# Kernel tuning notes

Hardware: AMD Instinct MI355X
Metric: run time of the kernel (lower is better)

The kernel has to match this reference:

```python
import jax, jax.numpy as jnp
import numpy as np

EPS = 1e-5
N_HEAD = 16


def layernorm(x, g, b):
    mu = jnp.mean(x, axis=-1, keepdims=True)
    var = jnp.mean(jnp.square(x - mu), axis=-1, keepdims=True)
    return (x - mu) * jax.lax.rsqrt(var + EPS) * g + b


def setup_inputs() -> dict:
    key = jax.random.key(0)
    ks = jax.random.split(key, 8)
    B, S, D = 4, 2048, 1024
    F = 4 * D
    s = 0.02
    return {
        "h": jax.random.normal(ks[0], (B, S, D), jnp.float32),
        "ln1_g": jnp.ones((D,), jnp.float32),
        "ln1_b": jnp.zeros((D,), jnp.float32),
        "wq": jax.random.normal(ks[1], (D, D), jnp.float32) * s,
        "bq": jnp.zeros((D,), jnp.float32),
        "wk": jax.random.normal(ks[2], (D, D), jnp.float32) * s,
        "bk": jnp.zeros((D,), jnp.float32),
        "wv": jax.random.normal(ks[3], (D, D), jnp.float32) * s,
        "bv": jnp.zeros((D,), jnp.float32),
        "wo": jax.random.normal(ks[4], (D, D), jnp.float32) * s,
        "bo": jnp.zeros((D,), jnp.float32),
        "ln2_g": jnp.ones((D,), jnp.float32),
        "ln2_b": jnp.zeros((D,), jnp.float32),
        "wfc": jax.random.normal(ks[5], (F, D), jnp.float32) * s,
        "bfc": jnp.zeros((F,), jnp.float32),
        "wproj": jax.random.normal(ks[6], (D, F), jnp.float32) * s,
        "bproj": jnp.zeros((D,), jnp.float32),
    }


def reference(h, ln1_g, ln1_b, wq, bq, wk, bk, wv, bv, wo, bo,
              ln2_g, ln2_b, wfc, bfc, wproj, bproj):
    B, S, D = h.shape
    H = N_HEAD
    Dh = D // H

    # --- attention sub-block ---
    r = h
    x = layernorm(h, ln1_g, ln1_b)
    q = (x @ wq.T + bq).reshape(B, S, H, Dh)
    k = (x @ wk.T + bk).reshape(B, S, H, Dh)
    v = (x @ wv.T + bv).reshape(B, S, H, Dh)

    scores = jnp.einsum("bqhd,bkhd->bhqk", q, k) / jnp.sqrt(jnp.float32(Dh))
    causal = jnp.tril(jnp.ones((S, S), bool))  # [S,S]
    scores = jnp.where(causal, scores, jnp.finfo(scores.dtype).min)
    probs = jax.nn.softmax(scores, axis=-1)
    o = jnp.einsum("bhqk,bkhd->bqhd", probs, v).reshape(B, S, D)
    h = r + (o @ wo.T + bo)

    # --- MLP sub-block ---
    r = h
    x = layernorm(h, ln2_g, ln2_b)
    x = jax.nn.gelu(x @ wfc.T + bfc, approximate=True)  # NewGELU (tanh)
    h = r + (x @ wproj.T + bproj)
    return h
```

## Files before the change

kernel.cpp:

```cpp
#include <hip/hip_runtime.h>
#include <hip/hip_bf16.h>
#include <stdint.h>


typedef short bf16x8 __attribute__((ext_vector_type(8)));
typedef float f32x4  __attribute__((ext_vector_type(4)));
typedef float f32x16 __attribute__((ext_vector_type(16)));
typedef short s16x4  __attribute__((ext_vector_type(4)));

__device__ __forceinline__ short f2bf(float f) {
  union { float f; uint32_t u; } a;
  a.f = f;
  uint32_t r = a.u + 0x7fffu + ((a.u >> 16) & 1u);
  return (short)(r >> 16);
}

__device__ __forceinline__ unsigned cvt_pk_bf16(float lo, float hi_) {
  unsigned r;
  asm("v_cvt_pk_bf16_f32 %0, %1, %2" : "=v"(r) : "v"(lo), "v"(hi_));
  return r;
}

__device__ __forceinline__ void gload_lds16(const void* g, void* l) {
  __builtin_amdgcn_global_load_lds(
      (const __attribute__((address_space(1))) void*)g,
      (__attribute__((address_space(3))) void*)l, 16, 0, 0);
}

__device__ __forceinline__ float gelu_f(float x) {
  float y = 0.7978845608028654f * (x + 0.044715f * x * x * x);
  y = fminf(fmaxf(y, -20.f), 20.f);
  float e = __expf(2.f * y);
  return 0.5f * x * (1.f + (e - 1.f) / (e + 1.f));
}

__global__ __launch_bounds__(256)
void cvt_f32_bf16(const float* __restrict__ in, short* __restrict__ out, int n4) {
  int i = blockIdx.x * 256 + threadIdx.x;
  if (i < n4) {
    float4 v = ((const float4*)in)[i];
    s16x4 o;
    o[0] = f2bf(v.x); o[1] = f2bf(v.y); o[2] = f2bf(v.z); o[3] = f2bf(v.w);
    ((s16x4*)out)[i] = o;
  }
}

__global__ __launch_bounds__(256)
void ln_fwd(const float* __restrict__ x, const float* __restrict__ g,
            const float* __restrict__ b, short* __restrict__ y) {
  const long row = blockIdx.x;
  const int t = threadIdx.x;
  const float4 xv = ((const float4*)(x + row * 1024))[t];
  float s  = xv.x + xv.y + xv.z + xv.w;
  float ss = xv.x * xv.x + xv.y * xv.y + xv.z * xv.z + xv.w * xv.w;
#pragma unroll
  for (int m = 1; m < 64; m <<= 1) {
    s  += __shfl_xor(s, m);
    ss += __shfl_xor(ss, m);
  }
  __shared__ float rs[4], rss[4];
  const int wid = t >> 6, lane = t & 63;
  if (lane == 0) { rs[wid] = s; rss[wid] = ss; }
  __syncthreads();
  s  = rs[0] + rs[1] + rs[2] + rs[3];
  ss = rss[0] + rss[1] + rss[2] + rss[3];
  const float mu   = s * (1.f / 1024.f);
  const float var  = ss * (1.f / 1024.f) - mu * mu;
  const float rstd = rsqrtf(var + 1e-5f);
  const float4 gv = ((const float4*)g)[t];
  const float4 bv = ((const float4*)b)[t];
  s16x4 ov;
  ov[0] = f2bf((xv.x - mu) * rstd * gv.x + bv.x);
  ov[1] = f2bf((xv.y - mu) * rstd * gv.y + bv.y);
  ov[2] = f2bf((xv.z - mu) * rstd * gv.z + bv.z);
  ov[3] = f2bf((xv.w - mu) * rstd * gv.w + bv.w);
  *(s16x4*)(y + row * 1024 + t * 4) = ov;
}

template <int OUT_BF16, int HAS_RES, int HAS_GELU>
__global__ __launch_bounds__(512, 2)
void gemm_bt2(const short* __restrict__ A, const short* __restrict__ W,
              const float* __restrict__ bias, const float* __restrict__ res,
              void* __restrict__ out, int M, int N, int K) {
  __shared__ short As[2][128 * 64];
  __shared__ short Bs[2][256 * 64];
  const int tid = threadIdx.x;
  const int wid = tid >> 6, lane = tid & 63;
  const int l16 = lane & 15, lg = lane >> 4;
  const int wm = wid >> 2, wn = wid & 3;

  const int nbx = N >> 8;
  const int nwg = nbx * (M >> 7);
  int flat = (int)blockIdx.x;
  if ((nwg & 7) == 0) flat = (flat & 7) * (nwg >> 3) + (flat >> 3);
  const int brow = (flat / nbx) * 128, bcol = (flat % nbx) * 256;

  f32x4 acc[4][4] = {};

  const int r0 = tid >> 3, g0 = tid & 7;

  auto STAGE = [&](int buf, int kt) {
#pragma unroll
    for (int i = 0; i < 2; ++i) {
      const int row = i * 64 + r0;
      gload_lds16(A + (long)(brow + row) * K + kt + 8 * (g0 ^ (row & 7)),
                  &As[buf][(i * 512 + wid * 64) * 8]);
    }
#pragma unroll
    for (int i = 0; i < 4; ++i) {
      const int row = i * 64 + r0;
      gload_lds16(W + (long)(bcol + row) * K + kt + 8 * (g0 ^ (row & 7)),
                  &Bs[buf][(i * 512 + wid * 64) * 8]);
    }
  };

  const int NT = K >> 6;
  STAGE(0, 0);
  STAGE(1, 64);

  for (int t = 0; t < NT; ++t) {
    const int cur = t & 1;
    if (t < NT - 1) asm volatile("s_waitcnt vmcnt(6)" ::: "memory");
    else            asm volatile("s_waitcnt vmcnt(0)" ::: "memory");
    __builtin_amdgcn_s_barrier();

    bf16x8 af0[4], af1[4], bf0[4], bf1[4];
#pragma unroll
    for (int m = 0; m < 4; ++m) {
      const int r = wm * 64 + m * 16 + l16;
      af0[m] = *(const bf16x8*)&As[cur][r * 64 + 8 * (lg ^ (r & 7))];
      af1[m] = *(const bf16x8*)&As[cur][r * 64 + 8 * ((4 + lg) ^ (r & 7))];
    }
#pragma unroll
    for (int n = 0; n < 4; ++n) {
      const int r = wn * 64 + n * 16 + l16;
      bf0[n] = *(const bf16x8*)&Bs[cur][r * 64 + 8 * (lg ^ (r & 7))];
      bf1[n] = *(const bf16x8*)&Bs[cur][r * 64 + 8 * ((4 + lg) ^ (r & 7))];
    }

    __builtin_amdgcn_s_setprio(1);
#pragma unroll
    for (int m = 0; m < 4; ++m)
#pragma unroll
      for (int n = 0; n < 4; ++n)
        acc[m][n] = __builtin_amdgcn_mfma_f32_16x16x32_bf16(af0[m], bf0[n], acc[m][n], 0, 0, 0);
    __builtin_amdgcn_s_setprio(0);

    asm volatile("s_waitcnt lgkmcnt(0)" ::: "memory");
    __builtin_amdgcn_s_barrier();
    if (t + 2 < NT) STAGE(cur, (t + 2) * 64);

    __builtin_amdgcn_s_setprio(1);
#pragma unroll
    for (int m = 0; m < 4; ++m)
#pragma unroll
      for (int n = 0; n < 4; ++n)
        acc[m][n] = __builtin_amdgcn_mfma_f32_16x16x32_bf16(af1[m], bf1[n], acc[m][n], 0, 0, 0);
    __builtin_amdgcn_s_setprio(0);
  }

#pragma unroll
  for (int n = 0; n < 4; ++n) {
    const int col = bcol + wn * 64 + n * 16 + l16;
    const float bb = bias[col];
#pragma unroll
    for (int m = 0; m < 4; ++m) {
#pragma unroll
      for (int j = 0; j < 4; ++j) {
        const long row = brow + wm * 64 + m * 16 + lg * 4 + j;
        float vv = acc[m][n][j] + bb;
        if (HAS_GELU) vv = gelu_f(vv);
        if (HAS_RES) vv += res[row * N + col];
        if (OUT_BF16) ((short*)out)[row * N + col] = f2bf(vv);
        else          ((float*)out)[row * N + col] = vv;
      }
    }
  }
}

__global__ __launch_bounds__(256)
void transpose_v(const short* __restrict__ v, short* __restrict__ vtg,
                 int S, int ldv, int H) {
  __shared__ short t[64][66];
  const int bh = blockIdx.y, b = bh / H, hh = bh % H;
  const int s0 = blockIdx.x * 64;
  const int tid = threadIdx.x;
#pragma unroll
  for (int i = 0; i < 2; ++i) {
    const int c = i * 256 + tid;
    const int sl = c >> 3, d8 = (c & 7) * 8;
    bf16x8 vv = *(const bf16x8*)&v[((long)b * S + s0 + sl) * ldv + hh * 64 + d8];
#pragma unroll
    for (int j = 0; j < 8; ++j) t[d8 + j][sl] = vv[j];
  }
  __syncthreads();
#pragma unroll
  for (int i = 0; i < 2; ++i) {
    const int c = i * 256 + tid;
    const int dl = c >> 3, s8 = (c & 7) * 8;
    bf16x8 ov;
#pragma unroll
    for (int j = 0; j < 8; ++j) ov[j] = t[dl][s8 + j];
    *(bf16x8*)&vtg[((long)bh * 64 + dl) * S + s0 + s8] = ov;
  }
}

__global__ __launch_bounds__(256, 4)
void attn_fwd2(const short* __restrict__ qg, const short* __restrict__ kg,
               const short* __restrict__ vtg, short* __restrict__ og,
               int S, int ldq, int D, int H) {
  const int tid = threadIdx.x, wid = tid >> 6, lane = tid & 63;
  const int l31 = lane & 31, hi = lane >> 5;
  const int fid = blockIdx.x;
  const int bh = fid & 63;
  const int b = bh / H, hh = bh % H;
  static const int perm[16] = {15, 0, 8, 7, 1, 14, 6, 9, 13, 2, 10, 5, 3, 12, 4, 11};
  const int qt = perm[(fid >> 6) & 15];
  const int q0 = qt * 128;
  const long qbase = (long)b * S * ldq + hh * 64;
  const long obase = (long)b * S * D + hh * 64;
  const long vbase = (long)bh * 64 * S;

  __shared__ short Ks[2][64 * 64];
  __shared__ short Vs[2][64 * 64];

  auto STAGE = [&](int buf, int k0) {
#pragma unroll
    for (int i = 0; i < 2; ++i) {
      const int c = i * 256 + tid;
      const int row = c >> 3, gl = c & 7;
      gload_lds16(&kg[qbase + (long)(k0 + row) * ldq + 8 * (gl ^ (row & 7))],
                  &Ks[buf][(i * 256 + wid * 64) * 8]);
      gload_lds16(&vtg[vbase + (long)row * S + k0 + 8 * (gl ^ (row & 7))],
                  &Vs[buf][(i * 256 + wid * 64) * 8]);
    }
  };

  const float kScale = 0.125f * 1.44269504089f;

  const int qw = q0 + wid * 32;
  const int qv = qw + l31;

  bf16x8 qf[4];
#pragma unroll
  for (int s = 0; s < 4; ++s)
    qf[s] = *(const bf16x8*)&qg[qbase + (long)qv * ldq + 16 * s + 8 * hi];

  f32x16 oa[2] = {};
  float mr = -3000.f, lr = 0.f;

  const int ntiles = qt * 2 + 2;

  STAGE(0, 0);
  for (int t = 0; t < ntiles; ++t) {
    const int cur = t & 1;
    const int k0 = t * 64;
    if (t + 1 < ntiles) {
      STAGE(cur ^ 1, k0 + 64);
      asm volatile("s_waitcnt vmcnt(4)" ::: "memory");
    } else {
      asm volatile("s_waitcnt vmcnt(0)" ::: "memory");
    }
    __builtin_amdgcn_s_barrier();

    if (k0 < qw + 32) {
      f32x16 st[2] = {};
#pragma unroll
      for (int s = 0; s < 4; ++s) {
        const int g = ((s << 1) | hi) ^ (l31 & 7);
        bf16x8 kf0 = *(const bf16x8*)&Ks[cur][l31 * 64 + 8 * g];
        bf16x8 kf1 = *(const bf16x8*)&Ks[cur][(32 + l31) * 64 + 8 * g];
        st[0] = __builtin_amdgcn_mfma_f32_32x32x16_bf16(kf0, qf[s], st[0], 0, 0, 0);
        st[1] = __builtin_amdgcn_mfma_f32_32x32x16_bf16(kf1, qf[s], st[1], 0, 0, 0);
      }

      const bool need_mask = (k0 + 63 > qw);
      float pv[2][16];
#pragma unroll
      for (int kb = 0; kb < 2; ++kb)
#pragma unroll
        for (int r = 0; r < 16; ++r) {
          float v = st[kb][r] * kScale;
          if (need_mask) {
            const int key = k0 + kb * 32 + (r & 3) + 8 * (r >> 2) + 4 * hi;
            if (key > qv) v = -1e30f;
          }
          pv[kb][r] = v;
        }

      float t8[8];
#pragma unroll
      for (int j = 0; j < 8; ++j)
        t8[j] = fmaxf(fmaxf(pv[0][j], pv[0][8 + j]), fmaxf(pv[1][j], pv[1][8 + j]));
      float rm = fmaxf(fmaxf(fmaxf(t8[0], t8[1]), fmaxf(t8[2], t8[3])),
                       fmaxf(fmaxf(t8[4], t8[5]), fmaxf(t8[6], t8[7])));
      rm = fmaxf(rm, __shfl_xor(rm, 32));

      const bool defer = (bool)__all(rm <= mr + 8.f);
      const float mn = defer ? mr : fmaxf(mr, rm);

      float a0 = 0.f, a1 = 0.f, a2 = 0.f, a3 = 0.f;
#pragma unroll
      for (int r = 0; r < 8; ++r) {
        float p0 = exp2f(pv[0][r] - mn);      pv[0][r] = p0;      a0 += p0;
        float p1 = exp2f(pv[0][8 + r] - mn);  pv[0][8 + r] = p1;  a1 += p1;
        float p2 = exp2f(pv[1][r] - mn);      pv[1][r] = p2;      a2 += p2;
        float p3 = exp2f(pv[1][8 + r] - mn);  pv[1][8 + r] = p3;  a3 += p3;
      }
      float ls = (a0 + a1) + (a2 + a3);
      ls += __shfl_xor(ls, 32);

      if (!defer) {
        const float alpha = exp2f(mr - mn);
        lr = lr * alpha + ls;
        mr = mn;
#pragma unroll
        for (int r = 0; r < 16; ++r) {
          const int crow = (r & 3) + 8 * (r >> 2) + 4 * hi;
          const float ar = __shfl(alpha, crow | (lane & 32));
          oa[0][r] *= ar;
          oa[1][r] *= ar;
        }
      } else {
        lr += ls;
      }

      bf16x8 pa[4];
#pragma unroll
      for (int kb = 0; kb < 2; ++kb) {
        unsigned pk[8], ex[8];
#pragma unroll
        for (int i2 = 0; i2 < 8; ++i2)
          pk[i2] = cvt_pk_bf16(pv[kb][2 * i2], pv[kb][2 * i2 + 1]);
#pragma unroll
        for (int i2 = 0; i2 < 8; ++i2)
          ex[i2] = (unsigned)__shfl_xor((int)pk[i2], 32);
        union { unsigned u[4]; bf16x8 v8; } f0, f1;
        f0.u[0] = hi ? ex[2] : pk[0];
        f0.u[1] = hi ? ex[3] : pk[1];
        f0.u[2] = hi ? pk[2] : ex[0];
        f0.u[3] = hi ? pk[3] : ex[1];
        f1.u[0] = hi ? ex[6] : pk[4];
        f1.u[1] = hi ? ex[7] : pk[5];
        f1.u[2] = hi ? pk[6] : ex[4];
        f1.u[3] = hi ? pk[7] : ex[5];
        pa[2 * kb]     = f0.v8;
        pa[2 * kb + 1] = f1.v8;
      }

#pragma unroll
      for (int s = 0; s < 4; ++s) {
        const int g = ((s << 1) | hi) ^ (l31 & 7);
        bf16x8 vf0 = *(const bf16x8*)&Vs[cur][l31 * 64 + 8 * g];
        bf16x8 vf1 = *(const bf16x8*)&Vs[cur][(32 + l31) * 64 + 8 * g];
        oa[0] = __builtin_amdgcn_mfma_f32_32x32x16_bf16(pa[s], vf0, oa[0], 0, 0, 0);
        oa[1] = __builtin_amdgcn_mfma_f32_32x32x16_bf16(pa[s], vf1, oa[1], 0, 0, 0);
      }
    }

    asm volatile("s_waitcnt lgkmcnt(0)" ::: "memory");
    __builtin_amdgcn_s_barrier();
  }

  const float linv = 1.f / lr;
#pragma unroll
  for (int r = 0; r < 16; ++r) {
    const int crow = (r & 3) + 8 * (r >> 2) + 4 * hi;
    const float li = __shfl(linv, crow | (lane & 32));
    const long row = qw + crow;
    og[obase + row * D + l31]      = f2bf(oa[0][r] * li);
    og[obase + row * D + 32 + l31] = f2bf(oa[1][r] * li);
  }
}

extern "C" void kernel_launch(void* const* d_in, const int* in_sizes, int n_in,
                              void* d_out, int out_size, void* d_ws, size_t ws_size,
                              hipStream_t stream) {
  (void)in_sizes; (void)n_in; (void)out_size; (void)ws_size;
  const float* h     = (const float*)d_in[0];
  const float* ln1_g = (const float*)d_in[1];
  const float* ln1_b = (const float*)d_in[2];
  const float* wq    = (const float*)d_in[3];
  const float* bq    = (const float*)d_in[4];
  const float* wk    = (const float*)d_in[5];
  const float* bk    = (const float*)d_in[6];
  const float* wv    = (const float*)d_in[7];
  const float* bv    = (const float*)d_in[8];
  const float* wo    = (const float*)d_in[9];
  const float* bo    = (const float*)d_in[10];
  const float* ln2_g = (const float*)d_in[11];
  const float* ln2_b = (const float*)d_in[12];
  const float* wfc   = (const float*)d_in[13];
  const float* bfc   = (const float*)d_in[14];
  const float* wproj = (const float*)d_in[15];
  const float* bproj = (const float*)d_in[16];

  const int B = 4, S = 2048, D = 1024, H = 16, F = 4096, T = B * S;
  const int D3 = 3 * D;

  char* ws = (char*)d_ws;
  size_t off = 0;
  auto alloc = [&](size_t bytes) {
    void* p = ws + off;
    off += (bytes + 255) & ~(size_t)255;
    return p;
  };
  short* xb   = (short*)alloc((size_t)T * D * 2);
  short* qkv  = (short*)alloc((size_t)T * D3 * 2);
  short* ob   = (short*)alloc((size_t)T * D * 2);
  float* h2   = (float*)alloc((size_t)T * D * 4);
  short* wqkvb  = (short*)alloc((size_t)D3 * D * 2);
  short* wob    = (short*)alloc((size_t)D * D * 2);
  short* wfcb   = (short*)alloc((size_t)F * D * 2);
  short* wprojb = (short*)alloc((size_t)D * F * 2);
  float* bqkv   = (float*)alloc((size_t)D3 * 4);
  short* ub  = qkv;
  short* vtg = (short*)h2;

  cvt_f32_bf16<<<dim3(D * D / 4 / 256), 256, 0, stream>>>(wq, wqkvb, D * D / 4);
  cvt_f32_bf16<<<dim3(D * D / 4 / 256), 256, 0, stream>>>(wk, wqkvb + (size_t)D * D, D * D / 4);
  cvt_f32_bf16<<<dim3(D * D / 4 / 256), 256, 0, stream>>>(wv, wqkvb + (size_t)2 * D * D, D * D / 4);
  cvt_f32_bf16<<<dim3(D * D / 4 / 256), 256, 0, stream>>>(wo, wob, D * D / 4);
  cvt_f32_bf16<<<dim3(F * D / 4 / 256), 256, 0, stream>>>(wfc, wfcb, F * D / 4);
  cvt_f32_bf16<<<dim3(D * F / 4 / 256), 256, 0, stream>>>(wproj, wprojb, D * F / 4);
  hipMemcpyAsync(bqkv,            bq, D * 4, hipMemcpyDeviceToDevice, stream);
  hipMemcpyAsync(bqkv + D,        bk, D * 4, hipMemcpyDeviceToDevice, stream);
  hipMemcpyAsync(bqkv + 2 * D,    bv, D * 4, hipMemcpyDeviceToDevice, stream);

  ln_fwd<<<dim3(T), 256, 0, stream>>>(h, ln1_g, ln1_b, xb);
  gemm_bt2<1, 0, 0><<<dim3((T / 128) * (D3 / 256)), 512, 0, stream>>>(
      xb, wqkvb, bqkv, nullptr, qkv, T, D3, D);
  transpose_v<<<dim3(S / 64, B * H), 256, 0, stream>>>(qkv + 2 * D, vtg, S, D3, H);
  attn_fwd2<<<dim3((S / 128) * (B * H / 64) * 64), 256, 0, stream>>>(
      qkv, qkv + D, vtg, ob, S, D3, D, H);
  gemm_bt2<0, 1, 0><<<dim3((T / 128) * (D / 256)), 512, 0, stream>>>(
      ob, wob, bo, h, h2, T, D, D);

  ln_fwd<<<dim3(T), 256, 0, stream>>>(h2, ln2_g, ln2_b, xb);
  gemm_bt2<1, 0, 1><<<dim3((T / 128) * (F / 256)), 512, 0, stream>>>(
      xb, wfcb, bfc, nullptr, ub, T, F, D);
  gemm_bt2<0, 1, 0><<<dim3((T / 128) * (D / 256)), 512, 0, stream>>>(
      ub, wprojb, bproj, h2, (float*)d_out, T, D, F);
}
```

Before: 415.6 us.

## Switch GEMM to triple-buffered K=32 stages with higher occupancy target

The GEMM K-tile shrinks from 64 to 32 and LDS staging moves from double to triple buffering, with the next-next tile issued at the start of each iteration. The launch bound now targets 4 workgroups per CU instead of 2, since LDS per block drops from 96KB to 72KB. The aim is to deepen prefetch and raise occupancy to hide global-load latency. In exchange there are twice as many barrier-synchronised iterations with half the MFMA work each, and register pressure rises under the tighter launch bound.

```diff
diff --git a/kernel.cpp b/kernel.cpp
--- a/kernel.cpp
+++ b/kernel.cpp
@@ -78,12 +78,12 @@
 }
 
 template <int OUT_BF16, int HAS_RES, int HAS_GELU>
-__global__ __launch_bounds__(512, 2)
-void gemm_bt2(const short* __restrict__ A, const short* __restrict__ W,
+__global__ __launch_bounds__(512, 4)
+void gemm_bt3(const short* __restrict__ A, const short* __restrict__ W,
               const float* __restrict__ bias, const float* __restrict__ res,
               void* __restrict__ out, int M, int N, int K) {
-  __shared__ short As[2][128 * 64];
-  __shared__ short Bs[2][256 * 64];
+  __shared__ short As[3][128 * 32];
+  __shared__ short Bs[3][256 * 32];
   const int tid = threadIdx.x;
   const int wid = tid >> 6, lane = tid & 63;
   const int l16 = lane & 15, lg = lane >> 4;
@@ -97,45 +97,46 @@
 
   f32x4 acc[4][4] = {};
 
-  const int r0 = tid >> 3, g0 = tid & 7;
+  const int r0 = tid >> 2, g0 = tid & 3;
 
   auto STAGE = [&](int buf, int kt) {
+    gload_lds16(A + (long)(brow + r0) * K + kt + 8 * (g0 ^ (r0 & 3)),
+                &As[buf][tid * 8]);
 #pragma unroll
     for (int i = 0; i < 2; ++i) {
-      const int row = i * 64 + r0;
-      gload_lds16(A + (long)(brow + row) * K + kt + 8 * (g0 ^ (row & 7)),
-                  &As[buf][(i * 512 + wid * 64) * 8]);
-    }
-#pragma unroll
-    for (int i = 0; i < 4; ++i) {
-      const int row = i * 64 + r0;
-      gload_lds16(W + (long)(bcol + row) * K + kt + 8 * (g0 ^ (row & 7)),
-                  &Bs[buf][(i * 512 + wid * 64) * 8]);
+      const int row = i * 128 + r0;
+      gload_lds16(W + (long)(bcol + row) * K + kt + 8 * (g0 ^ (row & 3)),
+                  &Bs[buf][(i * 512 + tid) * 8]);
     }
   };
 
-  const int NT = K >> 6;
+  const int NT = K >> 5;
   STAGE(0, 0);
-  STAGE(1, 64);
-
+  STAGE(1, 32);
+
+  int cur = 0;
   for (int t = 0; t < NT; ++t) {
-    const int cur = t & 1;
-    if (t < NT - 1) asm volatile("s_waitcnt vmcnt(6)" ::: "memory");
-    else            asm volatile("s_waitcnt vmcnt(0)" ::: "memory");
+    if (t + 2 < NT) {
+      int sb = cur + 2; if (sb >= 3) sb -= 3;
+      STAGE(sb, (t + 2) * 32);
+      asm volatile("s_waitcnt vmcnt(6)" ::: "memory");
+    } else if (t + 1 < NT) {
+      asm volatile("s_waitcnt vmcnt(3)" ::: "memory");
+    } else {
+      asm volatile("s_waitcnt vmcnt(0)" ::: "memory");
+    }
     __builtin_amdgcn_s_barrier();
 
-    bf16x8 af0[4], af1[4], bf0[4], bf1[4];
+    bf16x8 af[4], bf[4];
 #pragma unroll
     for (int m = 0; m < 4; ++m) {
       const int r = wm * 64 + m * 16 + l16;
-      af0[m] = *(const bf16x8*)&As[cur][r * 64 + 8 * (lg ^ (r & 7))];
-      af1[m] = *(const bf16x8*)&As[cur][r * 64 + 8 * ((4 + lg) ^ (r & 7))];
+      af[m] = *(const bf16x8*)&As[cur][r * 32 + 8 * (lg ^ (r & 3))];
     }
 #pragma unroll
     for (int n = 0; n < 4; ++n) {
       const int r = wn * 64 + n * 16 + l16;
-      bf0[n] = *(const bf16x8*)&Bs[cur][r * 64 + 8 * (lg ^ (r & 7))];
-      bf1[n] = *(const bf16x8*)&Bs[cur][r * 64 + 8 * ((4 + lg) ^ (r & 7))];
+      bf[n] = *(const bf16x8*)&Bs[cur][r * 32 + 8 * (lg ^ (r & 3))];
     }
 
     __builtin_amdgcn_s_setprio(1);
@@ -143,20 +144,12 @@
     for (int m = 0; m < 4; ++m)
 #pragma unroll
       for (int n = 0; n < 4; ++n)
-        acc[m][n] = __builtin_amdgcn_mfma_f32_16x16x32_bf16(af0[m], bf0[n], acc[m][n], 0, 0, 0);
+        acc[m][n] = __builtin_amdgcn_mfma_f32_16x16x32_bf16(af[m], bf[n], acc[m][n], 0, 0, 0);
     __builtin_amdgcn_s_setprio(0);
 
     asm volatile("s_waitcnt lgkmcnt(0)" ::: "memory");
     __builtin_amdgcn_s_barrier();
-    if (t + 2 < NT) STAGE(cur, (t + 2) * 64);
-
-    __builtin_amdgcn_s_setprio(1);
-#pragma unroll
-    for (int m = 0; m < 4; ++m)
-#pragma unroll
-      for (int n = 0; n < 4; ++n)
-        acc[m][n] = __builtin_amdgcn_mfma_f32_16x16x32_bf16(af1[m], bf1[n], acc[m][n], 0, 0, 0);
-    __builtin_amdgcn_s_setprio(0);
+    cur = (cur + 1 == 3) ? 0 : cur + 1;
   }
 
 #pragma unroll
@@ -428,17 +421,17 @@
   hipMemcpyAsync(bqkv + 2 * D,    bv, D * 4, hipMemcpyDeviceToDevice, stream);
 
   ln_fwd<<<dim3(T), 256, 0, stream>>>(h, ln1_g, ln1_b, xb);
-  gemm_bt2<1, 0, 0><<<dim3((T / 128) * (D3 / 256)), 512, 0, stream>>>(
+  gemm_bt3<1, 0, 0><<<dim3((T / 128) * (D3 / 256)), 512, 0, stream>>>(
       xb, wqkvb, bqkv, nullptr, qkv, T, D3, D);
   transpose_v<<<dim3(S / 64, B * H), 256, 0, stream>>>(qkv + 2 * D, vtg, S, D3, H);
   attn_fwd2<<<dim3((S / 128) * (B * H / 64) * 64), 256, 0, stream>>>(
       qkv, qkv + D, vtg, ob, S, D3, D, H);
-  gemm_bt2<0, 1, 0><<<dim3((T / 128) * (D / 256)), 512, 0, stream>>>(
+  gemm_bt3<0, 1, 0><<<dim3((T / 128) * (D / 256)), 512, 0, stream>>>(
       ob, wob, bo, h, h2, T, D, D);
 
   ln_fwd<<<dim3(T), 256, 0, stream>>>(h2, ln2_g, ln2_b, xb);
-  gemm_bt2<1, 0, 1><<<dim3((T / 128) * (F / 256)), 512, 0, stream>>>(
+  gemm_bt3<1, 0, 1><<<dim3((T / 128) * (F / 256)), 512, 0, stream>>>(
       xb, wfcb, bfc, nullptr, ub, T, F, D);
-  gemm_bt2<0, 1, 0><<<dim3((T / 128) * (D / 256)), 512, 0, stream>>>(
+  gemm_bt3<0, 1, 0><<<dim3((T / 128) * (D / 256)), 512, 0, stream>>>(
       ub, wprojb, bproj, h2, (float*)d_out, T, D, F);
 }
```

Result: slower. 440.2 us (+5.9%).

## Triple-buffer GEMM LDS staging and interleave global loads with MFMA halves

Applied to the files above, without the earlier changes.

The GEMM kernel moves from a double-buffered to a triple-buffered LDS pipeline. Global-to-LDS loads for tile t+2 are split across the two MFMA half-steps, with barriers and sched_barrier pinning the order so load issue overlaps compute. Fragment loads are reduced to one set of registers reused across both K halves. Launch bounds drop from 2 to 1 workgroup per CU because LDS use grows to 144KB, trading occupancy for a deeper prefetch pipeline.

```diff
diff --git a/kernel.cpp b/kernel.cpp
--- a/kernel.cpp
+++ b/kernel.cpp
@@ -78,12 +78,12 @@
 }
 
 template <int OUT_BF16, int HAS_RES, int HAS_GELU>
-__global__ __launch_bounds__(512, 2)
-void gemm_bt2(const short* __restrict__ A, const short* __restrict__ W,
+__global__ __launch_bounds__(512, 1)
+void gemm_bt4(const short* __restrict__ A, const short* __restrict__ W,
               const float* __restrict__ bias, const float* __restrict__ res,
               void* __restrict__ out, int M, int N, int K) {
-  __shared__ short As[2][128 * 64];
-  __shared__ short Bs[2][256 * 64];
+  __shared__ short As[3][128 * 64];
+  __shared__ short Bs[3][256 * 64];
   const int tid = threadIdx.x;
   const int wid = tid >> 6, lane = tid & 63;
   const int l16 = lane & 15, lg = lane >> 4;
@@ -99,64 +99,80 @@
 
   const int r0 = tid >> 3, g0 = tid & 7;
 
-  auto STAGE = [&](int buf, int kt) {
+  auto STAGE_A = [&](int buf, int kt) {
 #pragma unroll
     for (int i = 0; i < 2; ++i) {
       const int row = i * 64 + r0;
       gload_lds16(A + (long)(brow + row) * K + kt + 8 * (g0 ^ (row & 7)),
-                  &As[buf][(i * 512 + wid * 64) * 8]);
-    }
-#pragma unroll
-    for (int i = 0; i < 4; ++i) {
-      const int row = i * 64 + r0;
-      gload_lds16(W + (long)(bcol + row) * K + kt + 8 * (g0 ^ (row & 7)),
-                  &Bs[buf][(i * 512 + wid * 64) * 8]);
+                  &As[buf][(i * 512 + tid) * 8]);
     }
   };
+  auto STAGE_B = [&](int buf, int kt, int i) {
+    const int row = i * 64 + r0;
+    gload_lds16(W + (long)(bcol + row) * K + kt + 8 * (g0 ^ (row & 7)),
+                &Bs[buf][(i * 512 + tid) * 8]);
+  };
+
+  int ra[4], rb[4];
+#pragma unroll
+  for (int m = 0; m < 4; ++m) ra[m] = wm * 64 + m * 16 + l16;
+#pragma unroll
+  for (int n = 0; n < 4; ++n) rb[n] = wn * 64 + n * 16 + l16;
 
   const int NT = K >> 6;
-  STAGE(0, 0);
-  STAGE(1, 64);
-
+  STAGE_A(0, 0); STAGE_B(0, 0, 0); STAGE_B(0, 0, 1); STAGE_B(0, 0, 2); STAGE_B(0, 0, 3);
+  STAGE_A(1, 64); STAGE_B(1, 64, 0); STAGE_B(1, 64, 1); STAGE_B(1, 64, 2); STAGE_B(1, 64, 3);
+  asm volatile("s_waitcnt vmcnt(6)" ::: "memory");
+  __builtin_amdgcn_s_barrier();
+
+  int cur = 0;
   for (int t = 0; t < NT; ++t) {
-    const int cur = t & 1;
-    if (t < NT - 1) asm volatile("s_waitcnt vmcnt(6)" ::: "memory");
-    else            asm volatile("s_waitcnt vmcnt(0)" ::: "memory");
-    __builtin_amdgcn_s_barrier();
-
-    bf16x8 af0[4], af1[4], bf0[4], bf1[4];
-#pragma unroll
-    for (int m = 0; m < 4; ++m) {
-      const int r = wm * 64 + m * 16 + l16;
-      af0[m] = *(const bf16x8*)&As[cur][r * 64 + 8 * (lg ^ (r & 7))];
-      af1[m] = *(const bf16x8*)&As[cur][r * 64 + 8 * ((4 + lg) ^ (r & 7))];
-    }
-#pragma unroll
-    for (int n = 0; n < 4; ++n) {
-      const int r = wn * 64 + n * 16 + l16;
-      bf0[n] = *(const bf16x8*)&Bs[cur][r * 64 + 8 * (lg ^ (r & 7))];
-      bf1[n] = *(const bf16x8*)&Bs[cur][r * 64 + 8 * ((4 + lg) ^ (r & 7))];
-    }
-
+    const bool st = (t + 2 < NT);
+    int sb = cur + 2; if (sb >= 3) sb -= 3;
+    const int kt2 = (t + 2) << 6;
+
+    bf16x8 af[4], bf[4];
+#pragma unroll
+    for (int m = 0; m < 4; ++m)
+      af[m] = *(const bf16x8*)&As[cur][ra[m] * 64 + 8 * (lg ^ (ra[m] & 7))];
+#pragma unroll
+    for (int n = 0; n < 4; ++n)
+      bf[n] = *(const bf16x8*)&Bs[cur][rb[n] * 64 + 8 * (lg ^ (rb[n] & 7))];
+    if (st) { STAGE_A(sb, kt2); STAGE_B(sb, kt2, 0); }
+    __builtin_amdgcn_s_barrier();
+    asm volatile("s_waitcnt lgkmcnt(0)" ::: "memory");
+    __builtin_amdgcn_sched_barrier(0);
     __builtin_amdgcn_s_setprio(1);
 #pragma unroll
     for (int m = 0; m < 4; ++m)
 #pragma unroll
       for (int n = 0; n < 4; ++n)
-        acc[m][n] = __builtin_amdgcn_mfma_f32_16x16x32_bf16(af0[m], bf0[n], acc[m][n], 0, 0, 0);
+        acc[m][n] = __builtin_amdgcn_mfma_f32_16x16x32_bf16(af[m], bf[n], acc[m][n], 0, 0, 0);
     __builtin_amdgcn_s_setprio(0);
-
+    __builtin_amdgcn_s_barrier();
+
+#pragma unroll
+    for (int m = 0; m < 4; ++m)
+      af[m] = *(const bf16x8*)&As[cur][ra[m] * 64 + 8 * ((4 + lg) ^ (ra[m] & 7))];
+#pragma unroll
+    for (int n = 0; n < 4; ++n)
+      bf[n] = *(const bf16x8*)&Bs[cur][rb[n] * 64 + 8 * ((4 + lg) ^ (rb[n] & 7))];
+    if (st) { STAGE_B(sb, kt2, 1); STAGE_B(sb, kt2, 2); STAGE_B(sb, kt2, 3); }
+    __builtin_amdgcn_s_barrier();
     asm volatile("s_waitcnt lgkmcnt(0)" ::: "memory");
-    __builtin_amdgcn_s_barrier();
-    if (t + 2 < NT) STAGE(cur, (t + 2) * 64);
-
+    __builtin_amdgcn_sched_barrier(0);
     __builtin_amdgcn_s_setprio(1);
 #pragma unroll
     for (int m = 0; m < 4; ++m)
 #pragma unroll
       for (int n = 0; n < 4; ++n)
-        acc[m][n] = __builtin_amdgcn_mfma_f32_16x16x32_bf16(af1[m], bf1[n], acc[m][n], 0, 0, 0);
+        acc[m][n] = __builtin_amdgcn_mfma_f32_16x16x32_bf16(af[m], bf[n], acc[m][n], 0, 0, 0);
     __builtin_amdgcn_s_setprio(0);
+    if (t + 2 < NT)      asm volatile("s_waitcnt vmcnt(6)" ::: "memory");
+    else if (t + 1 < NT) asm volatile("s_waitcnt vmcnt(0)" ::: "memory");
+    __builtin_amdgcn_s_barrier();
+
+    cur = (cur + 1 == 3) ? 0 : cur + 1;
   }
 
 #pragma unroll
@@ -423,22 +439,22 @@
   cvt_f32_bf16<<<dim3(D * D / 4 / 256), 256, 0, stream>>>(wo, wob, D * D / 4);
   cvt_f32_bf16<<<dim3(F * D / 4 / 256), 256, 0, stream>>>(wfc, wfcb, F * D / 4);
   cvt_f32_bf16<<<dim3(D * F / 4 / 256), 256, 0, stream>>>(wproj, wprojb, D * F / 4);
-  hipMemcpyAsync(bqkv,            bq, D * 4, hipMemcpyDeviceToDevice, stream);
-  hipMemcpyAsync(bqkv + D,        bk, D * 4, hipMemcpyDeviceToDevice, stream);
-  hipMemcpyAsync(bqkv + 2 * D,    bv, D * 4, hipMemcpyDeviceToDevice, stream);
+  hipMemcpyAsync(bqkv,         bq, D * 4, hipMemcpyDeviceToDevice, stream);
+  hipMemcpyAsync(bqkv + D,     bk, D * 4, hipMemcpyDeviceToDevice, stream);
+  hipMemcpyAsync(bqkv + 2 * D, bv, D * 4, hipMemcpyDeviceToDevice, stream);
 
   ln_fwd<<<dim3(T), 256, 0, stream>>>(h, ln1_g, ln1_b, xb);
-  gemm_bt2<1, 0, 0><<<dim3((T / 128) * (D3 / 256)), 512, 0, stream>>>(
+  gemm_bt4<1, 0, 0><<<dim3((T / 128) * (D3 / 256)), 512, 0, stream>>>(
       xb, wqkvb, bqkv, nullptr, qkv, T, D3, D);
   transpose_v<<<dim3(S / 64, B * H), 256, 0, stream>>>(qkv + 2 * D, vtg, S, D3, H);
   attn_fwd2<<<dim3((S / 128) * (B * H / 64) * 64), 256, 0, stream>>>(
       qkv, qkv + D, vtg, ob, S, D3, D, H);
-  gemm_bt2<0, 1, 0><<<dim3((T / 128) * (D / 256)), 512, 0, stream>>>(
+  gemm_bt4<0, 1, 0><<<dim3((T / 128) * (D / 256)), 512, 0, stream>>>(
       ob, wob, bo, h, h2, T, D, D);
 
   ln_fwd<<<dim3(T), 256, 0, stream>>>(h2, ln2_g, ln2_b, xb);
-  gemm_bt2<1, 0, 1><<<dim3((T / 128) * (F / 256)), 512, 0, stream>>>(
+  gemm_bt4<1, 0, 1><<<dim3((T / 128) * (F / 256)), 512, 0, stream>>>(
       xb, wfcb, bfc, nullptr, ub, T, F, D);
-  gemm_bt2<0, 1, 0><<<dim3((T / 128) * (D / 256)), 512, 0, stream>>>(
+  gemm_bt4<0, 1, 0><<<dim3((T / 128) * (D / 256)), 512, 0, stream>>>(
       ub, wprojb, bproj, h2, (float*)d_out, T, D, F);
 }
```

Measured after the change: 401.6 us. -3.4%, faster.

## Replace double-buffered GEMM with single-buffer 4-wave kernel and fuse weight casts

Applied to the files above, without the earlier changes.

The GEMM moves from 8 waves with double-buffered LDS and explicit vmcnt pipelining to 4 waves per block, each computing a 64x128 sub-tile from a single LDS buffer with syncthreads around every K step. This gives more MFMA work per wave and uses half the LDS, but it drops the overlap between global loads and compute. Separately, the six weight-cast launches become one kernel that picks its source and destination by offset range, removing launch overhead.

```diff
diff --git a/kernel.cpp b/kernel.cpp
--- a/kernel.cpp
+++ b/kernel.cpp
@@ -34,14 +34,24 @@
   return 0.5f * x * (1.f + (e - 1.f) / (e + 1.f));
 }
 
+struct W6 {
+  const float* s[6];
+  short* d[6];
+  int off[7];
+};
+
 __global__ __launch_bounds__(256)
-void cvt_f32_bf16(const float* __restrict__ in, short* __restrict__ out, int n4) {
-  int i = blockIdx.x * 256 + threadIdx.x;
-  if (i < n4) {
-    float4 v = ((const float4*)in)[i];
-    s16x4 o;
-    o[0] = f2bf(v.x); o[1] = f2bf(v.y); o[2] = f2bf(v.z); o[3] = f2bf(v.w);
-    ((s16x4*)out)[i] = o;
+void cvt_all(W6 a) {
+  const int i = blockIdx.x * 256 + threadIdx.x;
+#pragma unroll
+  for (int k = 0; k < 6; ++k) {
+    if (i >= a.off[k] && i < a.off[k + 1]) {
+      const int j = i - a.off[k];
+      float4 v = ((const float4*)a.s[k])[j];
+      s16x4 o;
+      o[0] = f2bf(v.x); o[1] = f2bf(v.y); o[2] = f2bf(v.z); o[3] = f2bf(v.w);
+      ((s16x4*)a.d[k])[j] = o;
+    }
   }
 }
 
@@ -78,16 +88,16 @@
 }
 
 template <int OUT_BF16, int HAS_RES, int HAS_GELU>
-__global__ __launch_bounds__(512, 2)
-void gemm_bt2(const short* __restrict__ A, const short* __restrict__ W,
+__global__ __launch_bounds__(256, 2)
+void gemm_bt5(const short* __restrict__ A, const short* __restrict__ W,
               const float* __restrict__ bias, const float* __restrict__ res,
               void* __restrict__ out, int M, int N, int K) {
-  __shared__ short As[2][128 * 64];
-  __shared__ short Bs[2][256 * 64];
+  __shared__ short As[128 * 64];
+  __shared__ short Bs[256 * 64];
   const int tid = threadIdx.x;
   const int wid = tid >> 6, lane = tid & 63;
   const int l16 = lane & 15, lg = lane >> 4;
-  const int wm = wid >> 2, wn = wid & 3;
+  const int wm = wid >> 1, wn = wid & 1;
 
   const int nbx = N >> 8;
   const int nwg = nbx * (M >> 7);
@@ -95,73 +105,52 @@
   if ((nwg & 7) == 0) flat = (flat & 7) * (nwg >> 3) + (flat >> 3);
   const int brow = (flat / nbx) * 128, bcol = (flat % nbx) * 256;
 
-  f32x4 acc[4][4] = {};
+  f32x4 acc[4][8] = {};
 
   const int r0 = tid >> 3, g0 = tid & 7;
 
-  auto STAGE = [&](int buf, int kt) {
-#pragma unroll
-    for (int i = 0; i < 2; ++i) {
-      const int row = i * 64 + r0;
+  int ra[4], rb[8];
+#pragma unroll
+  for (int m = 0; m < 4; ++m) ra[m] = wm * 64 + m * 16 + l16;
+#pragma unroll
+  for (int n = 0; n < 8; ++n) rb[n] = wn * 128 + n * 16 + l16;
+
+  for (int kt = 0; kt < K; kt += 64) {
+    __syncthreads();
+#pragma unroll
+    for (int i = 0; i < 4; ++i) {
+      const int row = i * 32 + r0;
       gload_lds16(A + (long)(brow + row) * K + kt + 8 * (g0 ^ (row & 7)),
-                  &As[buf][(i * 512 + wid * 64) * 8]);
-    }
-#pragma unroll
-    for (int i = 0; i < 4; ++i) {
-      const int row = i * 64 + r0;
+                  &As[(i * 256 + tid) * 8]);
+    }
+#pragma unroll
+    for (int i = 0; i < 8; ++i) {
+      const int row = i * 32 + r0;
       gload_lds16(W + (long)(bcol + row) * K + kt + 8 * (g0 ^ (row & 7)),
-                  &Bs[buf][(i * 512 + wid * 64) * 8]);
-    }
-  };
-
-  const int NT = K >> 6;
-  STAGE(0, 0);
-  STAGE(1, 64);
-
-  for (int t = 0; t < NT; ++t) {
-    const int cur = t & 1;
-    if (t < NT - 1) asm volatile("s_waitcnt vmcnt(6)" ::: "memory");
-    else            asm volatile("s_waitcnt vmcnt(0)" ::: "memory");
-    __builtin_amdgcn_s_barrier();
-
-    bf16x8 af0[4], af1[4], bf0[4], bf1[4];
-#pragma unroll
-    for (int m = 0; m < 4; ++m) {
-      const int r = wm * 64 + m * 16 + l16;
-      af0[m] = *(const bf16x8*)&As[cur][r * 64 + 8 * (lg ^ (r & 7))];
-      af1[m] = *(const bf16x8*)&As[cur][r * 64 + 8 * ((4 + lg) ^ (r & 7))];
-    }
-#pragma unroll
-    for (int n = 0; n < 4; ++n) {
-      const int r = wn * 64 + n * 16 + l16;
-      bf0[n] = *(const bf16x8*)&Bs[cur][r * 64 + 8 * (lg ^ (r & 7))];
-      bf1[n] = *(const bf16x8*)&Bs[cur][r * 64 + 8 * ((4 + lg) ^ (r & 7))];
-    }
-
-    __builtin_amdgcn_s_setprio(1);
-#pragma unroll
-    for (int m = 0; m < 4; ++m)
-#pragma unroll
-      for (int n = 0; n < 4; ++n)
-        acc[m][n] = __builtin_amdgcn_mfma_f32_16x16x32_bf16(af0[m], bf0[n], acc[m][n], 0, 0, 0);
-    __builtin_amdgcn_s_setprio(0);
-
-    asm volatile("s_waitcnt lgkmcnt(0)" ::: "memory");
-    __builtin_amdgcn_s_barrier();
-    if (t + 2 < NT) STAGE(cur, (t + 2) * 64);
-
-    __builtin_amdgcn_s_setprio(1);
-#pragma unroll
-    for (int m = 0; m < 4; ++m)
-#pragma unroll
-      for (int n = 0; n < 4; ++n)
-        acc[m][n] = __builtin_amdgcn_mfma_f32_16x16x32_bf16(af1[m], bf1[n], acc[m][n], 0, 0, 0);
-    __builtin_amdgcn_s_setprio(0);
-  }
-
-#pragma unroll
-  for (int n = 0; n < 4; ++n) {
-    const int col = bcol + wn * 64 + n * 16 + l16;
+                  &Bs[(i * 256 + tid) * 8]);
+    }
+    __syncthreads();
+
+#pragma unroll
+    for (int kk = 0; kk < 2; ++kk) {
+      bf16x8 af[4], bf[8];
+#pragma unroll
+      for (int m = 0; m < 4; ++m)
+        af[m] = *(const bf16x8*)&As[ra[m] * 64 + 8 * ((kk * 4 + lg) ^ (ra[m] & 7))];
+#pragma unroll
+      for (int n = 0; n < 8; ++n)
+        bf[n] = *(const bf16x8*)&Bs[rb[n] * 64 + 8 * ((kk * 4 + lg) ^ (rb[n] & 7))];
+#pragma unroll
+      for (int m = 0; m < 4; ++m)
+#pragma unroll
+        for (int n = 0; n < 8; ++n)
+          acc[m][n] = __builtin_amdgcn_mfma_f32_16x16x32_bf16(af[m], bf[n], acc[m][n], 0, 0, 0);
+    }
+  }
+
+#pragma unroll
+  for (int n = 0; n < 8; ++n) {
+    const int col = bcol + wn * 128 + n * 16 + l16;
     const float bb = bias[col];
 #pragma unroll
     for (int m = 0; m < 4; ++m) {
@@ -417,28 +406,38 @@
   short* ub  = qkv;
   short* vtg = (short*)h2;
 
-  cvt_f32_bf16<<<dim3(D * D / 4 / 256), 256, 0, stream>>>(wq, wqkvb, D * D / 4);
-  cvt_f32_bf16<<<dim3(D * D / 4 / 256), 256, 0, stream>>>(wk, wqkvb + (size_t)D * D, D * D / 4);
-  cvt_f32_bf16<<<dim3(D * D / 4 / 256), 256, 0, stream>>>(wv, wqkvb + (size_t)2 * D * D, D * D / 4);
-  cvt_f32_bf16<<<dim3(D * D / 4 / 256), 256, 0, stream>>>(wo, wob, D * D / 4);
-  cvt_f32_bf16<<<dim3(F * D / 4 / 256), 256, 0, stream>>>(wfc, wfcb, F * D / 4);
-  cvt_f32_bf16<<<dim3(D * F / 4 / 256), 256, 0, stream>>>(wproj, wprojb, D * F / 4);
-  hipMemcpyAsync(bqkv,            bq, D * 4, hipMemcpyDeviceToDevice, stream);
-  hipMemcpyAsync(bqkv + D,        bk, D * 4, hipMemcpyDeviceToDevice, stream);
-  hipMemcpyAsync(bqkv + 2 * D,    bv, D * 4, hipMemcpyDeviceToDevice, stream);
+  W6 wargs;
+  const int nqq = D * D / 4;
+  wargs.s[0] = wq;    wargs.d[0] = wqkvb;
+  wargs.s[1] = wk;    wargs.d[1] = wqkvb + (size_t)D * D;
+  wargs.s[2] = wv;    wargs.d[2] = wqkvb + (size_t)2 * D * D;
+  wargs.s[3] = wo;    wargs.d[3] = wob;
+  wargs.s[4] = wfc;   wargs.d[4] = wfcb;
+  wargs.s[5] = wproj; wargs.d[5] = wprojb;
+  wargs.off[0] = 0;
+  wargs.off[1] = nqq;
+  wargs.off[2] = 2 * nqq;
+  wargs.off[3] = 3 * nqq;
+  wargs.off[4] = 4 * nqq;
+  wargs.off[5] = 4 * nqq + F * D / 4;
+  wargs.off[6] = 4 * nqq + 2 * (F * D / 4);
+  cvt_all<<<dim3(wargs.off[6] / 256), 256, 0, stream>>>(wargs);
+  hipMemcpyAsync(bqkv,         bq, D * 4, hipMemcpyDeviceToDevice, stream);
+  hipMemcpyAsync(bqkv + D,     bk, D * 4, hipMemcpyDeviceToDevice, stream);
+  hipMemcpyAsync(bqkv + 2 * D, bv, D * 4, hipMemcpyDeviceToDevice, stream);
 
   ln_fwd<<<dim3(T), 256, 0, stream>>>(h, ln1_g, ln1_b, xb);
-  gemm_bt2<1, 0, 0><<<dim3((T / 128) * (D3 / 256)), 512, 0, stream>>>(
+  gemm_bt5<1, 0, 0><<<dim3((T / 128) * (D3 / 256)), 256, 0, stream>>>(
       xb, wqkvb, bqkv, nullptr, qkv, T, D3, D);
   transpose_v<<<dim3(S / 64, B * H), 256, 0, stream>>>(qkv + 2 * D, vtg, S, D3, H);
   attn_fwd2<<<dim3((S / 128) * (B * H / 64) * 64), 256, 0, stream>>>(
       qkv, qkv + D, vtg, ob, S, D3, D, H);
-  gemm_bt2<0, 1, 0><<<dim3((T / 128) * (D / 256)), 512, 0, stream>>>(
+  gemm_bt5<0, 1, 0><<<dim3((T / 128) * (D / 256)), 256, 0, stream>>>(
       ob, wob, bo, h, h2, T, D, D);
 
   ln_fwd<<<dim3(T), 256, 0, stream>>>(h2, ln2_g, ln2_b, xb);
-  gemm_bt2<1, 0, 1><<<dim3((T / 128) * (F / 256)), 512, 0, stream>>>(
+  gemm_bt5<1, 0, 1><<<dim3((T / 128) * (F / 256)), 256, 0, stream>>>(
       xb, wfcb, bfc, nullptr, ub, T, F, D);
-  gemm_bt2<0, 1, 0><<<dim3((T / 128) * (D / 256)), 512, 0, stream>>>(
+  gemm_bt5<0, 1, 0><<<dim3((T / 128) * (D / 256)), 256, 0, stream>>>(
       ub, wprojb, bproj, h2, (float*)d_out, T, D, F);
 }
```

After: 402.8 us. 3.1% less time.
